# Performance work log

Measured on AMD Instinct MI355X. Metric: run time of the kernel, lower is better.

The kernel has to match this reference:

```python
import jax, jax.numpy as jnp
import numpy as np

B, XDIM, S = 32768, 32, 16
N_COMBINE = XDIM - 2  # 30 combines with out_channels=S (block0 + middle blocks)


def setup_inputs() -> dict:
    key = jax.random.key(0)
    k1, k2, k3, k4 = jax.random.split(key, 4)
    x = jax.random.randint(k1, (B, XDIM), 0, 2, dtype=jnp.int32)  # binary data
    leaf_logits = jax.random.normal(k2, (XDIM, S), dtype=jnp.float32)  # Bernoulli leaf logits per var
    sum_weights = jax.random.normal(k3, (N_COMBINE, S * S, S), dtype=jnp.float32)
    sum_weights_last = jax.random.normal(k4, (S * S, 1), dtype=jnp.float32)
    return {"x": x, "leaf_logits": leaf_logits, "sum_weights": sum_weights,
            "sum_weights_last": sum_weights_last}


def _combine(a, b, W):
    # a, b: [B, S] log-likelihoods; W: [S*S, OC] raw sum weights.
    # CrossProduct in log domain: out[:, i*S + j] = a[:, i] + b[:, j]
    cross = (a[:, :, None] + b[:, None, :]).reshape(a.shape[0], S * S)  # [B, S*S]
    logw = jax.nn.log_softmax(W, axis=0)  # normalize over in_channels
    # Sum node in log domain: logsumexp over input channels
    return jax.nn.logsumexp(cross[:, :, None] + logw[None, :, :], axis=1)  # [B, OC]


def reference(x, leaf_logits, sum_weights, sum_weights_last):
    xf = x.astype(jnp.float32)[:, :, None]  # [B, XDIM, 1]
    # Bernoulli leaf log-prob: x*log(sigmoid(l)) + (1-x)*log(1-sigmoid(l))
    lp = (xf * jax.nn.log_sigmoid(leaf_logits)[None]
          + (1.0 - xf) * jax.nn.log_sigmoid(-leaf_logits)[None])  # [B, XDIM, S]

    # block 0: combine leaves of vars 0 and 1
    curr = _combine(lp[:, 0], lp[:, 1], sum_weights[0])  # [B, S]

    # middle blocks: fold in vars 2 .. XDIM-2
    mid_leaves = jnp.swapaxes(lp[:, 2:XDIM - 1], 0, 1)  # [XDIM-3, B, S]

    def step(c, inp):
        leaf, W = inp
        return _combine(c, leaf, W), None

    curr, _ = jax.lax.scan(step, curr, (mid_leaves, sum_weights[1:]))

    # final block: fold in last var with out_channels=1 root sum
    out = _combine(curr, lp[:, XDIM - 1], sum_weights_last)  # [B, 1]
    return out[:, None, :]  # [B, 1, 1] to match torch output shape
```

## Files before the change

### kernel.cpp

```cpp
#include <hip/hip_runtime.h>

using uint = unsigned int;

#define DW_LO    0
#define DW_HIb   7616
#define DW_FT    15232
#define DW_DELTA 15360
#define DW_BASE  15392
#define DW_EB0   15396
#define DW_TOT   15616

template<int K>
__device__ __forceinline__ int roti(int x) {
    return __builtin_amdgcn_update_dpp(0, x, 0x120 | K, 0xF, 0xF, true);
}
template<int K>
__device__ __forceinline__ float rotf(float x) {
    return __builtin_bit_cast(float, roti<K>(__builtin_bit_cast(int, x)));
}
__device__ __forceinline__ float rowmax16(float d) {
    d = fmaxf(d, rotf<1>(d)); d = fmaxf(d, rotf<2>(d));
    d = fmaxf(d, rotf<4>(d)); d = fmaxf(d, rotf<8>(d));
    return d;
}
__device__ __forceinline__ float rowsum16(float d) {
    d += rotf<1>(d); d += rotf<2>(d); d += rotf<4>(d); d += rotf<8>(d);
    return d;
}
__device__ __forceinline__ float logsig(float z) {
    return fminf(z, 0.f) - log1pf(__expf(-fabsf(z)));
}
__device__ __forceinline__ uint bfpack(float a, float b) {
    uint ua = __builtin_bit_cast(uint, a);
    uint ub = __builtin_bit_cast(uint, b);
    ua = (ua + 0x7fffu + ((ua >> 16) & 1u)) >> 16;
    ub = ((ub + 0x7fffu + ((ub >> 16) & 1u)) >> 16) << 16;
    return ua | ub;
}
__device__ __forceinline__ float blo(uint u) { return __builtin_bit_cast(float, u << 16); }
__device__ __forceinline__ float bhi(uint u) { return __builtin_bit_cast(float, u & 0xffff0000u); }
__device__ __forceinline__ unsigned spread16(unsigned u) {
    u = (u | (u << 8)) & 0x00FF00FFu;
    u = (u | (u << 4)) & 0x0F0F0F0Fu;
    u = (u | (u << 2)) & 0x33333333u;
    u = (u | (u << 1)) & 0x55555555u;
    return u;
}

__global__ __launch_bounds__(1024) void prep(const float* __restrict__ sw,
                                             const float* __restrict__ swl,
                                             const float* __restrict__ ll,
                                             float* __restrict__ ws) {
    __shared__ __align__(16) float SW[16384];
    __shared__ float PM[1024];
    __shared__ float EB[128];
    __shared__ float CM[64], CS[64];
    __shared__ float CMl, CSl;
    __shared__ float WF[2048];
    __shared__ float T12[2048];
    __shared__ float MM[4096];
    __shared__ float WL[32];
    __shared__ float BMs[64];

    const int tid = threadIdx.x;
    const int t = blockIdx.x;
    const int lid = tid & 15;

    int s1 = roti<1>(lid) & 15,   s2 = roti<2>(lid) & 15,   s3 = roti<3>(lid) & 15;
    int s4 = roti<4>(lid) & 15,   s5 = roti<5>(lid) & 15,   s6 = roti<6>(lid) & 15;
    int s7 = roti<7>(lid) & 15,   s8 = roti<8>(lid) & 15,   s9 = roti<9>(lid) & 15;
    int s10 = roti<10>(lid) & 15, s11 = roti<11>(lid) & 15, s12 = roti<12>(lid) & 15;
    int s13 = roti<13>(lid) & 15, s14 = roti<14>(lid) & 15, s15 = roti<15>(lid) & 15;

    if (t < 7) {
        const float4* src = (const float4*)sw + t * 4096;
        #pragma unroll
        for (int k = 0; k < 4; ++k) ((float4*)SW)[tid + 1024 * k] = src[tid + 1024 * k];
        if (tid < 128) {
            int cc = tid >> 5, bb = (tid >> 4) & 1, var = 4 * t + 1 + cc;
            float l = ll[var * 16 + lid];
            float lp = bb ? logsig(l) : logsig(-l);
            EB[tid] = __expf(lp - rowmax16(lp));
        }
        __syncthreads();
        {
            int grp = tid >> 4, cc = grp >> 4, r = grp & 15;
            float m = -1e30f;
            #pragma unroll
            for (int q = 0; q < 16; ++q)
                m = fmaxf(m, SW[cc * 4096 + (r * 16 + q) * 16 + lid]);
            PM[grp * 16 + lid] = m;
        }
        __syncthreads();
        if (tid < 64) {
            int cc = tid >> 4, ocx = tid & 15;
            float m = -1e30f;
            #pragma unroll
            for (int r = 0; r < 16; ++r) m = fmaxf(m, PM[(cc * 16 + r) * 16 + ocx]);
            CM[tid] = m;
        }
        __syncthreads();
        {
            int base = tid * 16;
            const float* cmp = CM + ((tid >> 8) << 4);
            #pragma unroll
            for (int e = 0; e < 16; ++e) SW[base + e] = __expf(SW[base + e] - cmp[e]);
        }
        __syncthreads();
        {
            int grp = tid >> 4, cc = grp >> 4, r = grp & 15;
            float s = 0.f;
            #pragma unroll
            for (int q = 0; q < 16; ++q)
                s += SW[cc * 4096 + (r * 16 + q) * 16 + lid];
            PM[grp * 16 + lid] = s;
        }
        __syncthreads();
        if (tid < 64) {
            int cc = tid >> 4, ocx = tid & 15;
            float s = 0.f;
            #pragma unroll
            for (int r = 0; r < 16; ++r) s += PM[(cc * 16 + r) * 16 + ocx];
            CS[tid] = 1.0f / s;
        }
        __syncthreads();
        #pragma unroll
        for (int q = 0; q < 2; ++q) {
            int e = tid + q * 1024;
            int cb = e >> 8, cc = cb >> 1, i = (e >> 4) & 15, ocx = e & 15;
            float a = 0.f;
            #pragma unroll
            for (int j = 0; j < 16; ++j)
                a += EB[cb * 16 + j] * SW[cc * 4096 + i * 256 + j * 16 + ocx];
            WF[e] = a * CS[cc * 16 + ocx];
        }
        __syncthreads();
        {
            int bb = tid >> 8, i = (tid >> 4) & 15, l = lid;
            float a = 0.f, a2 = 0.f;
            #pragma unroll
            for (int k = 0; k < 16; ++k) {
                a  += WF[(bb & 1) * 256 + i * 16 + k]       * WF[(2 + (bb >> 1)) * 256 + k * 16 + l];
                a2 += WF[(4 + (bb & 1)) * 256 + i * 16 + k] * WF[(6 + (bb >> 1)) * 256 + k * 16 + l];
            }
            T12[tid] = a;
            T12[1024 + tid] = a2;
        }
        __syncthreads();
        #pragma unroll
        for (int q = 0; q < 4; ++q) {
            int e = tid + q * 1024;
            int v = e >> 8, i = (e >> 4) & 15, ocx = e & 15;
            float a = 0.f;
            #pragma unroll
            for (int k = 0; k < 16; ++k)
                a += T12[(v & 3) * 256 + i * 16 + k] * T12[1024 + (v >> 2) * 256 + k * 16 + ocx];
            MM[e] = a;
        }
        __syncthreads();
        if (tid < 256) {
            int v = tid >> 4, ocx = lid;
            const float* m = MM + v * 256;
            float x0 = m[ocx * 16 + ocx];
            float x1 = m[s1 * 16 + ocx],   x2 = m[s2 * 16 + ocx],   x3 = m[s3 * 16 + ocx];
            float x4 = m[s4 * 16 + ocx],   x5 = m[s5 * 16 + ocx],   x6 = m[s6 * 16 + ocx];
            float x7 = m[s7 * 16 + ocx],   x8 = m[s8 * 16 + ocx],   x9 = m[s9 * 16 + ocx];
            float x10 = m[s10 * 16 + ocx], x11 = m[s11 * 16 + ocx], x12 = m[s12 * 16 + ocx];
            float x13 = m[s13 * 16 + ocx], x14 = m[s14 * 16 + ocx], x15 = m[s15 * 16 + ocx];
            uint4 lo4, hi4;
            lo4.x = bfpack(x0, x1);   lo4.y = bfpack(x2, x3);
            lo4.z = bfpack(x4, x5);   lo4.w = bfpack(x6, x7);
            hi4.x = bfpack(x8, x9);   hi4.y = bfpack(x10, x11);
            hi4.z = bfpack(x12, x13); hi4.w = bfpack(x14, x15);
            uint* wsu = (uint*)ws;
            int dw = t * 1088 + v * 68 + ocx * 4;
            *(uint4*)(wsu + dw) = lo4;
            *(uint4*)(wsu + DW_HIb + dw) = hi4;
        }
    } else {
        const float4* s28 = (const float4*)(sw + 28 * 4096);
        #pragma unroll
        for (int k = 0; k < 2; ++k) ((float4*)SW)[tid + 1024 * k] = s28[tid + 1024 * k];
        if (tid < 64) ((float4*)SW)[2048 + tid] = ((const float4*)swl)[tid];
        if (tid < 96) {
            int cb = tid >> 4, bb = cb & 1;
            int var = (cb < 4) ? (29 + (cb >> 1)) : 31;
            float l = ll[var * 16 + lid];
            float lp = bb ? logsig(l) : logsig(-l);
            EB[tid] = __expf(lp - rowmax16(lp));
        }
        __syncthreads();
        {
            int grp = tid >> 4;
            if (grp < 32) {
                int cc = grp >> 4, r = grp & 15;
                float m = -1e30f;
                #pragma unroll
                for (int q = 0; q < 16; ++q)
                    m = fmaxf(m, SW[cc * 4096 + (r * 16 + q) * 16 + lid]);
                PM[grp * 16 + lid] = m;
            } else if (grp == 32) {
                float m = -1e30f;
                #pragma unroll
                for (int q = 0; q < 16; ++q) m = fmaxf(m, SW[8192 + q * 16 + lid]);
                m = rowmax16(m);
                if (lid == 0) CMl = m;
            }
        }
        __syncthreads();
        if (tid < 32) {
            int cc = tid >> 4, ocx = tid & 15;
            float m = -1e30f;
            #pragma unroll
            for (int r = 0; r < 16; ++r) m = fmaxf(m, PM[(cc * 16 + r) * 16 + ocx]);
            CM[tid] = m;
        }
        __syncthreads();
        for (int idx = tid; idx < 8448; idx += 1024) {
            float cm = (idx < 8192) ? CM[((idx >> 12) << 4) | (idx & 15)] : CMl;
            SW[idx] = __expf(SW[idx] - cm);
        }
        __syncthreads();
        {
            int grp = tid >> 4;
            if (grp < 32) {
                int cc = grp >> 4, r = grp & 15;
                float s = 0.f;
                #pragma unroll
                for (int q = 0; q < 16; ++q)
                    s += SW[cc * 4096 + (r * 16 + q) * 16 + lid];
                PM[grp * 16 + lid] = s;
            } else if (grp == 32) {
                float s = 0.f;
                #pragma unroll
                for (int q = 0; q < 16; ++q) s += SW[8192 + q * 16 + lid];
                s = rowsum16(s);
                if (lid == 0) CSl = 1.0f / s;
            }
        }
        __syncthreads();
        if (tid < 32) {
            int cc = tid >> 4, ocx = tid & 15;
            float s = 0.f;
            #pragma unroll
            for (int r = 0; r < 16; ++r) s += PM[(cc * 16 + r) * 16 + ocx];
            CS[tid] = 1.0f / s;
        }
        __syncthreads();
        {
            int cb = tid >> 8, cc = cb >> 1, i = (tid >> 4) & 15, ocx = lid;
            float a = 0.f;
            #pragma unroll
            for (int j = 0; j < 16; ++j)
                a += EB[cb * 16 + j] * SW[cc * 4096 + i * 256 + j * 16 + ocx];
            WF[tid] = a * CS[cc * 16 + ocx];
        }
        if (tid < 32) {
            int bb = tid >> 4;
            float a = 0.f;
            #pragma unroll
            for (int j = 0; j < 16; ++j)
                a += EB[(4 + bb) * 16 + j] * SW[8192 + lid * 16 + j];
            WL[tid] = a * CSl;
        }
        __syncthreads();
        {
            int b01 = tid >> 8, i = (tid >> 4) & 15, l = lid;
            float a = 0.f;
            #pragma unroll
            for (int k = 0; k < 16; ++k)
                a += WF[(b01 & 1) * 256 + i * 16 + k] * WF[(2 + (b01 >> 1)) * 256 + k * 16 + l];
            T12[tid] = a;
        }
        __syncthreads();
        if (tid < 128) {
            int v = tid >> 4;
            float a = 0.f;
            #pragma unroll
            for (int l = 0; l < 16; ++l)
                a += T12[(v & 3) * 256 + lid * 16 + l] * WL[(v >> 2) * 16 + l];
            ws[DW_FT + v * 16 + lid] = a;
        }
        if (tid >= 128 && tid < 192) {
            int u = tid - 128, var = u >> 1, bb = u & 1;
            float m = -1e30f;
            #pragma unroll
            for (int j = 0; j < 16; ++j) {
                float l = ll[var * 16 + j];
                m = fmaxf(m, bb ? logsig(l) : logsig(-l));
            }
            BMs[u] = m;
        }
        if (tid >= 192 && tid < 224) {
            int u = tid - 192, bb = u >> 4, j = u & 15;
            float m = -1e30f;
            #pragma unroll
            for (int jj = 0; jj < 16; ++jj) {
                float l = ll[jj];
                m = fmaxf(m, bb ? logsig(l) : logsig(-l));
            }
            float l = ll[j];
            ws[DW_EB0 + u] = __expf((bb ? logsig(l) : logsig(-l)) - m);
        }
        __syncthreads();
        if (tid < 32) ws[DW_DELTA + tid] = BMs[2 * tid + 1] - BMs[2 * tid];
        if (tid >= 64 && tid < 128) {
            int u = tid - 64;
            float vb = (u < 32) ? BMs[2 * u] : 0.f;
            #pragma unroll
            for (int off = 32; off >= 1; off >>= 1) vb += __shfl_xor(vb, off);
            if (u == 0) ws[DW_BASE] = vb;
        }
    }
}

__device__ __forceinline__ float quadstep(const uint* sPT, float acc, int dw) {
    uint4 wl4 = *(const uint4*)(sPT + dw);
    uint4 wh4 = *(const uint4*)(sPT + DW_HIb + dw);
    float d0 = acc * blo(wl4.x);
    d0 = fmaf(rotf<1>(acc), bhi(wl4.x), d0);
    d0 = fmaf(rotf<2>(acc), blo(wl4.y), d0);
    d0 = fmaf(rotf<3>(acc), bhi(wl4.y), d0);
    d0 = fmaf(rotf<4>(acc), blo(wl4.z), d0);
    d0 = fmaf(rotf<5>(acc), bhi(wl4.z), d0);
    d0 = fmaf(rotf<6>(acc), blo(wl4.w), d0);
    d0 = fmaf(rotf<7>(acc), bhi(wl4.w), d0);
    float d1 = rotf<8>(acc) * blo(wh4.x);
    d1 = fmaf(rotf<9>(acc),  bhi(wh4.x), d1);
    d1 = fmaf(rotf<10>(acc), blo(wh4.y), d1);
    d1 = fmaf(rotf<11>(acc), bhi(wh4.y), d1);
    d1 = fmaf(rotf<12>(acc), blo(wh4.z), d1);
    d1 = fmaf(rotf<13>(acc), bhi(wh4.z), d1);
    d1 = fmaf(rotf<14>(acc), blo(wh4.w), d1);
    d1 = fmaf(rotf<15>(acc), bhi(wh4.w), d1);
    return d0 + d1;
}

__global__ __launch_bounds__(512, 4) void spn_main(const int* __restrict__ x,
                                                   const float* __restrict__ ws,
                                                   float* __restrict__ out) {
    __shared__ __align__(16) float sL[DW_TOT];
    const int tid = threadIdx.x;
    const int g = tid >> 4, oc = tid & 15;
    const int b0 = blockIdx.x * 64 + g;
    const int b1 = b0 + 32;

    int2 xa = *(const int2*)(x + b0 * 32 + 2 * oc);
    int2 xb = *(const int2*)(x + b1 * 32 + 2 * oc);
    unsigned long long ma0 = __ballot(xa.x & 1);
    unsigned long long ma1 = __ballot(xa.y & 1);
    unsigned long long mb0 = __ballot(xb.x & 1);
    unsigned long long mb1 = __ballot(xb.y & 1);
    const int gw = g & 3;
    unsigned bitsA = spread16((unsigned)(ma0 >> (gw * 16)) & 0xffffu)
                   | (spread16((unsigned)(ma1 >> (gw * 16)) & 0xffffu) << 1);
    unsigned bitsB = spread16((unsigned)(mb0 >> (gw * 16)) & 0xffffu)
                   | (spread16((unsigned)(mb1 >> (gw * 16)) & 0xffffu) << 1);

    for (int k = tid; k < DW_TOT / 4; k += 512)
        ((float4*)sL)[k] = ((const float4*)ws)[k];
    __syncthreads();

    float2 dl = *(const float2*)(sL + DW_DELTA + 2 * oc);
    float pa = ((xa.x & 1) ? dl.x : 0.f) + ((xa.y & 1) ? dl.y : 0.f);
    float pb = ((xb.x & 1) ? dl.x : 0.f) + ((xb.y & 1) ? dl.y : 0.f);
    float base = sL[DW_BASE];
    float LA = base + rowsum16(pa);
    float LB = base + rowsum16(pb);

    float accA = sL[DW_EB0 + (bitsA & 1) * 16 + oc];
    float accB = sL[DW_EB0 + (bitsB & 1) * 16 + oc];
    const uint* sPT = (const uint*)sL;
    const int ocd = oc * 4;

    #pragma unroll
    for (int p = 0; p < 7; ++p) {
        int dwA = p * 1088 + (int)((bitsA >> (4 * p + 1)) & 15) * 68 + ocd;
        int dwB = p * 1088 + (int)((bitsB >> (4 * p + 1)) & 15) * 68 + ocd;
        float dA = quadstep(sPT, accA, dwA);
        float dB = quadstep(sPT, accB, dwB);
        if (p & 1) {
            float mA = rowmax16(dA), mB = rowmax16(dB);
            accA = dA * __builtin_amdgcn_rcpf(mA);
            accB = dB * __builtin_amdgcn_rcpf(mB);
            LA += __logf(mA);
            LB += __logf(mB);
        } else {
            accA = dA; accB = dB;
        }
    }

    float tsA = rowsum16(accA * sL[DW_FT + ((bitsA >> 29) & 7) * 16 + oc]);
    float tsB = rowsum16(accB * sL[DW_FT + ((bitsB >> 29) & 7) * 16 + oc]);
    if (oc == 0) {
        out[b0] = LA + __logf(tsA);
        out[b1] = LB + __logf(tsB);
    }
}

extern "C" void kernel_launch(void* const* d_in, const int* in_sizes, int n_in,
                              void* d_out, int out_size, void* d_ws, size_t ws_size,
                              hipStream_t stream) {
    const int*   x   = (const int*)d_in[0];
    const float* ll  = (const float*)d_in[1];
    const float* sw  = (const float*)d_in[2];
    const float* swl = (const float*)d_in[3];
    float* out = (float*)d_out;
    float* ws  = (float*)d_ws;

    hipLaunchKernelGGL(prep,     dim3(8),   dim3(1024), 0, stream, sw, swl, ll, ws);
    hipLaunchKernelGGL(spn_main, dim3(512), dim3(512),  0, stream, x, ws, out);
}
```

Baseline: 23.49 us.

## Split weight prep into per-combine normalization kernel and DPP-based matrix-chain kernel

```diff
diff --git a/kernel.cpp b/kernel.cpp
--- a/kernel.cpp
+++ b/kernel.cpp
@@ -9,6 +9,8 @@
 #define DW_BASE  15392
 #define DW_EB0   15396
 #define DW_TOT   15616
+#define WFW      16384
+#define WLW      31744
 
 template<int K>
 __device__ __forceinline__ int roti(int x) {
@@ -47,120 +49,199 @@
     return u;
 }
 
-__global__ __launch_bounds__(1024) void prep(const float* __restrict__ sw,
+__global__ __launch_bounds__(256) void prep1(const float* __restrict__ sw,
                                              const float* __restrict__ swl,
                                              const float* __restrict__ ll,
                                              float* __restrict__ ws) {
-    __shared__ __align__(16) float SW[16384];
-    __shared__ float PM[1024];
-    __shared__ float EB[128];
-    __shared__ float CM[64], CS[64];
-    __shared__ float CMl, CSl;
-    __shared__ float WF[2048];
-    __shared__ float T12[2048];
-    __shared__ float MM[4096];
-    __shared__ float WL[32];
+    __shared__ float pm[256];
+    __shared__ float ebs[32];
     __shared__ float BMs[64];
-
     const int tid = threadIdx.x;
-    const int t = blockIdx.x;
-    const int lid = tid & 15;
-
-    int s1 = roti<1>(lid) & 15,   s2 = roti<2>(lid) & 15,   s3 = roti<3>(lid) & 15;
-    int s4 = roti<4>(lid) & 15,   s5 = roti<5>(lid) & 15,   s6 = roti<6>(lid) & 15;
-    int s7 = roti<7>(lid) & 15,   s8 = roti<8>(lid) & 15,   s9 = roti<9>(lid) & 15;
-    int s10 = roti<10>(lid) & 15, s11 = roti<11>(lid) & 15, s12 = roti<12>(lid) & 15;
-    int s13 = roti<13>(lid) & 15, s14 = roti<14>(lid) & 15, s15 = roti<15>(lid) & 15;
-
-    if (t < 7) {
-        const float4* src = (const float4*)sw + t * 4096;
-        #pragma unroll
-        for (int k = 0; k < 4; ++k) ((float4*)SW)[tid + 1024 * k] = src[tid + 1024 * k];
-        if (tid < 128) {
-            int cc = tid >> 5, bb = (tid >> 4) & 1, var = 4 * t + 1 + cc;
-            float l = ll[var * 16 + lid];
+    const int c = blockIdx.x;
+    const int i = tid >> 4, oc = tid & 15;
+
+    if (c < 30) {
+        if (tid < 32) {
+            int bb = tid >> 4;
+            float l = ll[(c + 1) * 16 + oc];
             float lp = bb ? logsig(l) : logsig(-l);
-            EB[tid] = __expf(lp - rowmax16(lp));
-        }
-        __syncthreads();
+            ebs[tid] = __expf(lp - rowmax16(lp));
+        }
+        const float* Wb = sw + c * 4096;
+        float w[16]; float m = -1e30f;
+        #pragma unroll
+        for (int j = 0; j < 16; ++j) {
+            w[j] = Wb[i * 256 + j * 16 + oc];
+            m = fmaxf(m, w[j]);
+        }
+        pm[i * 16 + oc] = m;
+        __syncthreads();
+        float cm = pm[oc];
+        #pragma unroll
+        for (int r = 1; r < 16; ++r) cm = fmaxf(cm, pm[r * 16 + oc]);
+        float e[16]; float s = 0.f;
+        #pragma unroll
+        for (int j = 0; j < 16; ++j) { e[j] = __expf(w[j] - cm); s += e[j]; }
+        __syncthreads();
+        pm[i * 16 + oc] = s;
+        __syncthreads();
+        float ss = pm[oc];
+        #pragma unroll
+        for (int r = 1; r < 16; ++r) ss += pm[r * 16 + oc];
+        float inv = 1.0f / ss;
+        float a0 = 0.f, a1 = 0.f;
+        #pragma unroll
+        for (int j = 0; j < 16; ++j) { a0 += ebs[j] * e[j]; a1 += ebs[16 + j] * e[j]; }
+        ws[WFW + ((c * 2 + 0) * 16 + i) * 16 + oc] = a0 * inv;
+        ws[WFW + ((c * 2 + 1) * 16 + i) * 16 + oc] = a1 * inv;
+    } else {
+        float v = swl[tid];
+        float m = v;
+        #pragma unroll
+        for (int off = 32; off >= 1; off >>= 1) m = fmaxf(m, __shfl_xor(m, off));
+        if ((tid & 63) == 0) pm[tid >> 6] = m;
+        if (tid < 32) {
+            int bb = tid >> 4;
+            float l = ll[31 * 16 + oc];
+            float lp = bb ? logsig(l) : logsig(-l);
+            ebs[tid] = __expf(lp - rowmax16(lp));
+        }
+        __syncthreads();
+        m = fmaxf(fmaxf(pm[0], pm[1]), fmaxf(pm[2], pm[3]));
+        float e = __expf(v - m);
+        float s = e;
+        #pragma unroll
+        for (int off = 32; off >= 1; off >>= 1) s += __shfl_xor(s, off);
+        __syncthreads();
+        if ((tid & 63) == 0) pm[tid >> 6] = s;
+        __syncthreads();
+        float inv = 1.0f / (pm[0] + pm[1] + pm[2] + pm[3]);
+        float t0 = rowsum16(ebs[oc] * e);
+        float t1 = rowsum16(ebs[16 + oc] * e);
+        if (oc == 0) {
+            ws[WLW + 0 + i]  = t0 * inv;
+            ws[WLW + 16 + i] = t1 * inv;
+        }
+        if (tid < 64) {
+            int var = tid >> 1, bb = tid & 1;
+            float mm_ = -1e30f;
+            #pragma unroll
+            for (int j = 0; j < 16; ++j) {
+                float l = ll[var * 16 + j];
+                mm_ = fmaxf(mm_, bb ? logsig(l) : logsig(-l));
+            }
+            BMs[tid] = mm_;
+        }
+        if (tid >= 64 && tid < 96) {
+            int u = tid - 64, bb = u >> 4, j = u & 15;
+            float mm_ = -1e30f;
+            #pragma unroll
+            for (int jj = 0; jj < 16; ++jj) {
+                float l = ll[jj];
+                mm_ = fmaxf(mm_, bb ? logsig(l) : logsig(-l));
+            }
+            float l = ll[j];
+            ws[DW_EB0 + u] = __expf((bb ? logsig(l) : logsig(-l)) - mm_);
+        }
+        __syncthreads();
+        if (tid < 32) ws[DW_DELTA + tid] = BMs[2 * tid + 1] - BMs[2 * tid];
+        if (tid < 64) {
+            float vb = (tid < 32) ? BMs[2 * tid] : 0.f;
+            #pragma unroll
+            for (int off = 32; off >= 1; off >>= 1) vb += __shfl_xor(vb, off);
+            if (tid == 0) ws[DW_BASE] = vb;
+        }
+    }
+}
+
+__global__ __launch_bounds__(256) void prep2(float* __restrict__ ws) {
+    __shared__ __align__(16) float WFs[2048];
+    __shared__ float Ts[1024];
+    __shared__ float Ms[4096];
+    const int tid = threadIdx.x;
+    const int p = blockIdx.x;
+    const int i = tid >> 4, oc = tid & 15;
+
+    int s1 = roti<1>(oc) & 15,   s2 = roti<2>(oc) & 15,   s3 = roti<3>(oc) & 15;
+    int s4 = roti<4>(oc) & 15,   s5 = roti<5>(oc) & 15,   s6 = roti<6>(oc) & 15;
+    int s7 = roti<7>(oc) & 15,   s8 = roti<8>(oc) & 15,   s9 = roti<9>(oc) & 15;
+    int s10 = roti<10>(oc) & 15, s11 = roti<11>(oc) & 15, s12 = roti<12>(oc) & 15;
+    int s13 = roti<13>(oc) & 15, s14 = roti<14>(oc) & 15, s15 = roti<15>(oc) & 15;
+    int sidx[16] = {oc, s1, s2, s3, s4, s5, s6, s7, s8, s9, s10, s11, s12, s13, s14, s15};
+
+    if (p < 7) {
+        const float4* src = (const float4*)(ws + WFW + p * 2048);
+        ((float4*)WFs)[tid]       = src[tid];
+        ((float4*)WFs)[256 + tid] = src[256 + tid];
+        __syncthreads();
+
+        float wf0[2], wf2[2];
+        wf0[0] = WFs[0 * 256 + i * 16 + oc];
+        wf0[1] = WFs[1 * 256 + i * 16 + oc];
+        wf2[0] = WFs[4 * 256 + i * 16 + oc];
+        wf2[1] = WFs[5 * 256 + i * 16 + oc];
+
+        float t1[4], t2[4];
         {
-            int grp = tid >> 4, cc = grp >> 4, r = grp & 15;
-            float m = -1e30f;
+            float w10 = WFs[2 * 256 + oc * 16 + oc], w11 = WFs[3 * 256 + oc * 16 + oc];
+            float w30 = WFs[6 * 256 + oc * 16 + oc], w31 = WFs[7 * 256 + oc * 16 + oc];
+            t1[0] = wf0[0] * w10; t1[1] = wf0[1] * w10;
+            t1[2] = wf0[0] * w11; t1[3] = wf0[1] * w11;
+            t2[0] = wf2[0] * w30; t2[1] = wf2[1] * w30;
+            t2[2] = wf2[0] * w31; t2[3] = wf2[1] * w31;
+        }
+        #define QSTEP(T) { \
+            float r0 = rotf<T>(wf0[0]), r1 = rotf<T>(wf0[1]); \
+            float w10 = WFs[2 * 256 + sidx[T] * 16 + oc], w11 = WFs[3 * 256 + sidx[T] * 16 + oc]; \
+            t1[0] = fmaf(r0, w10, t1[0]); t1[1] = fmaf(r1, w10, t1[1]); \
+            t1[2] = fmaf(r0, w11, t1[2]); t1[3] = fmaf(r1, w11, t1[3]); \
+            float q0 = rotf<T>(wf2[0]), q1 = rotf<T>(wf2[1]); \
+            float w30 = WFs[6 * 256 + sidx[T] * 16 + oc], w31 = WFs[7 * 256 + sidx[T] * 16 + oc]; \
+            t2[0] = fmaf(q0, w30, t2[0]); t2[1] = fmaf(q1, w30, t2[1]); \
+            t2[2] = fmaf(q0, w31, t2[2]); t2[3] = fmaf(q1, w31, t2[3]); }
+        QSTEP(1) QSTEP(2) QSTEP(3) QSTEP(4) QSTEP(5) QSTEP(6) QSTEP(7) QSTEP(8)
+        QSTEP(9) QSTEP(10) QSTEP(11) QSTEP(12) QSTEP(13) QSTEP(14) QSTEP(15)
+        #undef QSTEP
+
+        #pragma unroll
+        for (int b = 0; b < 4; ++b) Ts[b * 256 + i * 16 + oc] = t2[b];
+        __syncthreads();
+
+        float M[16];
+        {
+            float c0 = Ts[0 * 256 + oc * 16 + oc], c1 = Ts[1 * 256 + oc * 16 + oc];
+            float c2 = Ts[2 * 256 + oc * 16 + oc], c3 = Ts[3 * 256 + oc * 16 + oc];
             #pragma unroll
-            for (int q = 0; q < 16; ++q)
-                m = fmaxf(m, SW[cc * 4096 + (r * 16 + q) * 16 + lid]);
-            PM[grp * 16 + lid] = m;
-        }
-        __syncthreads();
-        if (tid < 64) {
-            int cc = tid >> 4, ocx = tid & 15;
-            float m = -1e30f;
-            #pragma unroll
-            for (int r = 0; r < 16; ++r) m = fmaxf(m, PM[(cc * 16 + r) * 16 + ocx]);
-            CM[tid] = m;
-        }
-        __syncthreads();
+            for (int b12 = 0; b12 < 4; ++b12) {
+                M[b12 + 0]  = t1[b12] * c0;
+                M[b12 + 4]  = t1[b12] * c1;
+                M[b12 + 8]  = t1[b12] * c2;
+                M[b12 + 12] = t1[b12] * c3;
+            }
+        }
+        #define MSTEP(T) { \
+            float c0 = Ts[0 * 256 + sidx[T] * 16 + oc], c1 = Ts[1 * 256 + sidx[T] * 16 + oc]; \
+            float c2 = Ts[2 * 256 + sidx[T] * 16 + oc], c3 = Ts[3 * 256 + sidx[T] * 16 + oc]; \
+            float r0 = rotf<T>(t1[0]), r1 = rotf<T>(t1[1]), r2 = rotf<T>(t1[2]), r3 = rotf<T>(t1[3]); \
+            M[0]  = fmaf(r0, c0, M[0]);  M[1]  = fmaf(r1, c0, M[1]); \
+            M[2]  = fmaf(r2, c0, M[2]);  M[3]  = fmaf(r3, c0, M[3]); \
+            M[4]  = fmaf(r0, c1, M[4]);  M[5]  = fmaf(r1, c1, M[5]); \
+            M[6]  = fmaf(r2, c1, M[6]);  M[7]  = fmaf(r3, c1, M[7]); \
+            M[8]  = fmaf(r0, c2, M[8]);  M[9]  = fmaf(r1, c2, M[9]); \
+            M[10] = fmaf(r2, c2, M[10]); M[11] = fmaf(r3, c2, M[11]); \
+            M[12] = fmaf(r0, c3, M[12]); M[13] = fmaf(r1, c3, M[13]); \
+            M[14] = fmaf(r2, c3, M[14]); M[15] = fmaf(r3, c3, M[15]); }
+        MSTEP(1) MSTEP(2) MSTEP(3) MSTEP(4) MSTEP(5) MSTEP(6) MSTEP(7) MSTEP(8)
+        MSTEP(9) MSTEP(10) MSTEP(11) MSTEP(12) MSTEP(13) MSTEP(14) MSTEP(15)
+        #undef MSTEP
+
+        #pragma unroll
+        for (int v = 0; v < 16; ++v) Ms[v * 256 + i * 16 + oc] = M[v];
+        __syncthreads();
+
         {
-            int base = tid * 16;
-            const float* cmp = CM + ((tid >> 8) << 4);
-            #pragma unroll
-            for (int e = 0; e < 16; ++e) SW[base + e] = __expf(SW[base + e] - cmp[e]);
-        }
-        __syncthreads();
-        {
-            int grp = tid >> 4, cc = grp >> 4, r = grp & 15;
-            float s = 0.f;
-            #pragma unroll
-            for (int q = 0; q < 16; ++q)
-                s += SW[cc * 4096 + (r * 16 + q) * 16 + lid];
-            PM[grp * 16 + lid] = s;
-        }
-        __syncthreads();
-        if (tid < 64) {
-            int cc = tid >> 4, ocx = tid & 15;
-            float s = 0.f;
-            #pragma unroll
-            for (int r = 0; r < 16; ++r) s += PM[(cc * 16 + r) * 16 + ocx];
-            CS[tid] = 1.0f / s;
-        }
-        __syncthreads();
-        #pragma unroll
-        for (int q = 0; q < 2; ++q) {
-            int e = tid + q * 1024;
-            int cb = e >> 8, cc = cb >> 1, i = (e >> 4) & 15, ocx = e & 15;
-            float a = 0.f;
-            #pragma unroll
-            for (int j = 0; j < 16; ++j)
-                a += EB[cb * 16 + j] * SW[cc * 4096 + i * 256 + j * 16 + ocx];
-            WF[e] = a * CS[cc * 16 + ocx];
-        }
-        __syncthreads();
-        {
-            int bb = tid >> 8, i = (tid >> 4) & 15, l = lid;
-            float a = 0.f, a2 = 0.f;
-            #pragma unroll
-            for (int k = 0; k < 16; ++k) {
-                a  += WF[(bb & 1) * 256 + i * 16 + k]       * WF[(2 + (bb >> 1)) * 256 + k * 16 + l];
-                a2 += WF[(4 + (bb & 1)) * 256 + i * 16 + k] * WF[(6 + (bb >> 1)) * 256 + k * 16 + l];
-            }
-            T12[tid] = a;
-            T12[1024 + tid] = a2;
-        }
-        __syncthreads();
-        #pragma unroll
-        for (int q = 0; q < 4; ++q) {
-            int e = tid + q * 1024;
-            int v = e >> 8, i = (e >> 4) & 15, ocx = e & 15;
-            float a = 0.f;
-            #pragma unroll
-            for (int k = 0; k < 16; ++k)
-                a += T12[(v & 3) * 256 + i * 16 + k] * T12[1024 + (v >> 2) * 256 + k * 16 + ocx];
-            MM[e] = a;
-        }
-        __syncthreads();
-        if (tid < 256) {
-            int v = tid >> 4, ocx = lid;
-            const float* m = MM + v * 256;
+            int v = i, ocx = oc;
+            const float* m = Ms + v * 256;
             float x0 = m[ocx * 16 + ocx];
             float x1 = m[s1 * 16 + ocx],   x2 = m[s2 * 16 + ocx],   x3 = m[s3 * 16 + ocx];
             float x4 = m[s4 * 16 + ocx],   x5 = m[s5 * 16 + ocx],   x6 = m[s6 * 16 + ocx];
@@ -173,143 +254,38 @@
             hi4.x = bfpack(x8, x9);   hi4.y = bfpack(x10, x11);
             hi4.z = bfpack(x12, x13); hi4.w = bfpack(x14, x15);
             uint* wsu = (uint*)ws;
-            int dw = t * 1088 + v * 68 + ocx * 4;
+            int dw = p * 1088 + v * 68 + ocx * 4;
             *(uint4*)(wsu + dw) = lo4;
             *(uint4*)(wsu + DW_HIb + dw) = hi4;
         }
     } else {
-        const float4* s28 = (const float4*)(sw + 28 * 4096);
-        #pragma unroll
-        for (int k = 0; k < 2; ++k) ((float4*)SW)[tid + 1024 * k] = s28[tid + 1024 * k];
-        if (tid < 64) ((float4*)SW)[2048 + tid] = ((const float4*)swl)[tid];
-        if (tid < 96) {
-            int cb = tid >> 4, bb = cb & 1;
-            int var = (cb < 4) ? (29 + (cb >> 1)) : 31;
-            float l = ll[var * 16 + lid];
-            float lp = bb ? logsig(l) : logsig(-l);
-            EB[tid] = __expf(lp - rowmax16(lp));
-        }
-        __syncthreads();
+        const float4* src = (const float4*)(ws + WFW + 28 * 512);
+        ((float4*)WFs)[tid] = src[tid];
+        __syncthreads();
+
+        float wf28[2];
+        wf28[0] = WFs[0 * 256 + i * 16 + oc];
+        wf28[1] = WFs[1 * 256 + i * 16 + oc];
+        float t01[4];
         {
-            int grp = tid >> 4;
-            if (grp < 32) {
-                int cc = grp >> 4, r = grp & 15;
-                float m = -1e30f;
-                #pragma unroll
-                for (int q = 0; q < 16; ++q)
-                    m = fmaxf(m, SW[cc * 4096 + (r * 16 + q) * 16 + lid]);
-                PM[grp * 16 + lid] = m;
-            } else if (grp == 32) {
-                float m = -1e30f;
-                #pragma unroll
-                for (int q = 0; q < 16; ++q) m = fmaxf(m, SW[8192 + q * 16 + lid]);
-                m = rowmax16(m);
-                if (lid == 0) CMl = m;
-            }
-        }
-        __syncthreads();
-        if (tid < 32) {
-            int cc = tid >> 4, ocx = tid & 15;
-            float m = -1e30f;
-            #pragma unroll
-            for (int r = 0; r < 16; ++r) m = fmaxf(m, PM[(cc * 16 + r) * 16 + ocx]);
-            CM[tid] = m;
-        }
-        __syncthreads();
-        for (int idx = tid; idx < 8448; idx += 1024) {
-            float cm = (idx < 8192) ? CM[((idx >> 12) << 4) | (idx & 15)] : CMl;
-            SW[idx] = __expf(SW[idx] - cm);
-        }
-        __syncthreads();
-        {
-            int grp = tid >> 4;
-            if (grp < 32) {
-                int cc = grp >> 4, r = grp & 15;
-                float s = 0.f;
-                #pragma unroll
-                for (int q = 0; q < 16; ++q)
-                    s += SW[cc * 4096 + (r * 16 + q) * 16 + lid];
-                PM[grp * 16 + lid] = s;
-            } else if (grp == 32) {
-                float s = 0.f;
-                #pragma unroll
-                for (int q = 0; q < 16; ++q) s += SW[8192 + q * 16 + lid];
-                s = rowsum16(s);
-                if (lid == 0) CSl = 1.0f / s;
-            }
-        }
-        __syncthreads();
-        if (tid < 32) {
-            int cc = tid >> 4, ocx = tid & 15;
-            float s = 0.f;
-            #pragma unroll
-            for (int r = 0; r < 16; ++r) s += PM[(cc * 16 + r) * 16 + ocx];
-            CS[tid] = 1.0f / s;
-        }
-        __syncthreads();
-        {
-            int cb = tid >> 8, cc = cb >> 1, i = (tid >> 4) & 15, ocx = lid;
-            float a = 0.f;
-            #pragma unroll
-            for (int j = 0; j < 16; ++j)
-                a += EB[cb * 16 + j] * SW[cc * 4096 + i * 256 + j * 16 + ocx];
-            WF[tid] = a * CS[cc * 16 + ocx];
-        }
-        if (tid < 32) {
-            int bb = tid >> 4;
-            float a = 0.f;
-            #pragma unroll
-            for (int j = 0; j < 16; ++j)
-                a += EB[(4 + bb) * 16 + j] * SW[8192 + lid * 16 + j];
-            WL[tid] = a * CSl;
-        }
-        __syncthreads();
-        {
-            int b01 = tid >> 8, i = (tid >> 4) & 15, l = lid;
-            float a = 0.f;
-            #pragma unroll
-            for (int k = 0; k < 16; ++k)
-                a += WF[(b01 & 1) * 256 + i * 16 + k] * WF[(2 + (b01 >> 1)) * 256 + k * 16 + l];
-            T12[tid] = a;
-        }
-        __syncthreads();
-        if (tid < 128) {
-            int v = tid >> 4;
-            float a = 0.f;
-            #pragma unroll
-            for (int l = 0; l < 16; ++l)
-                a += T12[(v & 3) * 256 + lid * 16 + l] * WL[(v >> 2) * 16 + l];
-            ws[DW_FT + v * 16 + lid] = a;
-        }
-        if (tid >= 128 && tid < 192) {
-            int u = tid - 128, var = u >> 1, bb = u & 1;
-            float m = -1e30f;
-            #pragma unroll
-            for (int j = 0; j < 16; ++j) {
-                float l = ll[var * 16 + j];
-                m = fmaxf(m, bb ? logsig(l) : logsig(-l));
-            }
-            BMs[u] = m;
-        }
-        if (tid >= 192 && tid < 224) {
-            int u = tid - 192, bb = u >> 4, j = u & 15;
-            float m = -1e30f;
-            #pragma unroll
-            for (int jj = 0; jj < 16; ++jj) {
-                float l = ll[jj];
-                m = fmaxf(m, bb ? logsig(l) : logsig(-l));
-            }
-            float l = ll[j];
-            ws[DW_EB0 + u] = __expf((bb ? logsig(l) : logsig(-l)) - m);
-        }
-        __syncthreads();
-        if (tid < 32) ws[DW_DELTA + tid] = BMs[2 * tid + 1] - BMs[2 * tid];
-        if (tid >= 64 && tid < 128) {
-            int u = tid - 64;
-            float vb = (u < 32) ? BMs[2 * u] : 0.f;
-            #pragma unroll
-            for (int off = 32; off >= 1; off >>= 1) vb += __shfl_xor(vb, off);
-            if (u == 0) ws[DW_BASE] = vb;
+            float w0 = WFs[2 * 256 + oc * 16 + oc], w1 = WFs[3 * 256 + oc * 16 + oc];
+            t01[0] = wf28[0] * w0; t01[1] = wf28[1] * w0;
+            t01[2] = wf28[0] * w1; t01[3] = wf28[1] * w1;
+        }
+        #define FSTEP(T) { \
+            float r0 = rotf<T>(wf28[0]), r1 = rotf<T>(wf28[1]); \
+            float w0 = WFs[2 * 256 + sidx[T] * 16 + oc], w1 = WFs[3 * 256 + sidx[T] * 16 + oc]; \
+            t01[0] = fmaf(r0, w0, t01[0]); t01[1] = fmaf(r1, w0, t01[1]); \
+            t01[2] = fmaf(r0, w1, t01[2]); t01[3] = fmaf(r1, w1, t01[3]); }
+        FSTEP(1) FSTEP(2) FSTEP(3) FSTEP(4) FSTEP(5) FSTEP(6) FSTEP(7) FSTEP(8)
+        FSTEP(9) FSTEP(10) FSTEP(11) FSTEP(12) FSTEP(13) FSTEP(14) FSTEP(15)
+        #undef FSTEP
+
+        float wl0 = ws[WLW + oc], wl1 = ws[WLW + 16 + oc];
+        #pragma unroll
+        for (int v = 0; v < 8; ++v) {
+            float f = rowsum16(t01[v & 3] * ((v >> 2) ? wl1 : wl0));
+            if (oc == 0) ws[DW_FT + v * 16 + i] = f;
         }
     }
 }
@@ -408,6 +384,7 @@
     float* out = (float*)d_out;
     float* ws  = (float*)d_ws;
 
-    hipLaunchKernelGGL(prep,     dim3(8),   dim3(1024), 0, stream, sw, swl, ll, ws);
-    hipLaunchKernelGGL(spn_main, dim3(512), dim3(512),  0, stream, x, ws, out);
-}
+    hipLaunchKernelGGL(prep1,    dim3(31),  dim3(256), 0, stream, sw, swl, ll, ws);
+    hipLaunchKernelGGL(prep2,    dim3(8),   dim3(256), 0, stream, ws);
+    hipLaunchKernelGGL(spn_main, dim3(512), dim3(512), 0, stream, x, ws, out);
+}
```

Result: slower. 24.83 us (+5.7%).
